# Optimization experiments

Measured on AMD Instinct MI355X. Metric: run time of the kernel, lower is better.

## Reference

```python
import jax, jax.numpy as jnp
import numpy as np


def setup_inputs() -> dict:
    key = jax.random.key(0)
    k1, k2, k3, k4, k5 = jax.random.split(key, 5)
    N, C, H, W = 1, 256, 336, 336
    R, P = 256, 7
    features = jax.random.normal(k1, (N, C, H, W), dtype=jnp.float32)
    # ROIs: integer [x1, y1, x2, y2]; width/height in [P, 63] so every bin is non-empty,
    # and boxes stay inside the feature map.
    x1 = jax.random.randint(k2, (R,), 0, H - 64)
    y1 = jax.random.randint(k3, (R,), 0, H - 64)
    w = jax.random.randint(k4, (R,), P, 64)
    h = jax.random.randint(k5, (R,), P, 64)
    rois = jnp.stack([x1, y1, x1 + w, y1 + h], axis=1).astype(jnp.int32)
    return {"features": features, "rois": rois, "output_size": P}


def _bin_index(lo, size, P, L):
    """For each roi, map every coordinate in [0, L) to its bin index in [0, P), or P if outside.

    Boundaries replicate: int(x1 + (width / P) * w) with float32 division and
    truncation (coords are non-negative, so trunc == floor).
    lo, size: [R] float32.  Returns [R, L] int32.
    """
    ws = jnp.arange(P + 1, dtype=jnp.float32)
    b = jnp.floor(lo[:, None] + (size / P)[:, None] * ws[None, :]).astype(jnp.int32)  # [R, P+1]
    j = jnp.arange(L, dtype=jnp.int32)
    # bin index = number of interior boundaries b[1..P] that are <= j
    cnt = jnp.sum((j[None, None, :] >= b[:, 1:, None]).astype(jnp.int32), axis=1)  # [R, L]
    return jnp.where(j[None, :] < b[:, :1], P, cnt)


def reference(features, rois, output_size):
    P = output_size
    feat = features[0]  # [C, H, W]  (original code requires N == 1)
    C, H, W = feat.shape
    x1 = rois[:, 0].astype(jnp.float32)
    y1 = rois[:, 1].astype(jnp.float32)
    rw = jnp.maximum(rois[:, 2] - rois[:, 0] + 1, 1).astype(jnp.float32)
    rh = jnp.maximum(rois[:, 3] - rois[:, 1] + 1, 1).astype(jnp.float32)
    col_bin = _bin_index(x1, rw, P, W)  # [R, W]
    row_bin = _bin_index(y1, rh, P, H)  # [R, H]

    def pool_one(cb, rb):
        # reduce columns into width-bins: [W, C, H] -> [P+1, C, H], drop 'outside' segment
        t = jax.ops.segment_max(jnp.moveaxis(feat, 2, 0), cb, num_segments=P + 1)[:P]  # [Pw, C, H]
        # reduce rows into height-bins: [H, Pw, C] -> [P+1, Pw, C]
        t = jax.ops.segment_max(jnp.moveaxis(t, 2, 0), rb, num_segments=P + 1)[:P]  # [Ph, Pw, C]
        return jnp.transpose(t, (2, 0, 1))  # [C, Ph, Pw]

    return jax.vmap(pool_one)(col_bin, row_bin)  # [R, C, P, P]
```

## Files before the change

kernel.cpp:

```cpp
#include <hip/hip_runtime.h>
#include <math.h>


#define POOL_P 7

__device__ __forceinline__ float4 max4(float4 a, float4 b) {
  return make_float4(fmaxf(a.x, b.x), fmaxf(a.y, b.y),
                     fmaxf(a.z, b.z), fmaxf(a.w, b.w));
}

__global__ __launch_bounds__(128) void roipool_kernel(
    const float* __restrict__ feat, const int* __restrict__ rois,
    float* __restrict__ out, int C, int H, int W, int R) {
  const int x  = blockIdx.x & 7;
  const int s  = blockIdx.x >> 3;
  const int pass = s / R;
  const int r    = s - pass * R;
  const int cg8  = (pass << 3) | x;

  const int wid  = threadIdx.x >> 6;
  const int lane = threadIdx.x & 63;
  const int k  = lane >> 4;
  const int li = lane & 15;
  const int c0 = (cg8 << 3) + (wid << 2);

  const int4 roi = *reinterpret_cast<const int4*>(rois + 4 * r);
  const int x1 = roi.x, y1 = roi.y;
  const int rw = max(roi.z - x1 + 1, 1);
  const int rh = max(roi.w - y1 + 1, 1);
  const int x2 = x1 + rw - 1;

  const float sx = __fdiv_rn((float)rw, (float)POOL_P);
  const float sy = __fdiv_rn((float)rh, (float)POOL_P);
  const float x1f = (float)x1, y1f = (float)y1;

  const int xa = x1 & ~3;
  const bool tailc = (x2 >= xa + 64);

  const int lslot = min((x2 - xa) >> 2, 15);
  const int lic = min(li, lslot);

  const size_t HW = (size_t)H * W;
  const float* fck = feat + (size_t)(c0 + k) * HW;
  const float* pm  = fck + xa + (lic << 2);
  const float* pt  = fck + xa + 64;

  __shared__ float stg[2][POOL_P][4][72];
  extern __shared__ float lds_pad[];

  const float NEG = -__builtin_inff();

#pragma unroll
  for (int ph = 0; ph < POOL_P; ++ph) {
    const int h0   = (int)__fadd_rn(y1f, __fmul_rn(sy, (float)ph));
    const int hend = (int)__fadd_rn(y1f, __fmul_rn(sy, (float)(ph + 1)));
    const int hl = hend - 1;
    float4 m  = make_float4(NEG, NEG, NEG, NEG);
    float4 tm = m;
    for (int h = h0; h < hend; h += 4) {
      const int o1 = (min(h + 1, hl) - h) * W;
      const int o2 = (min(h + 2, hl) - h) * W;
      const int o3 = (min(h + 3, hl) - h) * W;
      const float* p = pm + (size_t)h * W;
      float4 v0 = *reinterpret_cast<const float4*>(p);
      float4 v1 = *reinterpret_cast<const float4*>(p + o1);
      float4 v2 = *reinterpret_cast<const float4*>(p + o2);
      float4 v3 = *reinterpret_cast<const float4*>(p + o3);
      m = max4(m, max4(max4(v0, v1), max4(v2, v3)));
      if (tailc && li == 0) {
        const float* q = pt + (size_t)h * W;
        float4 t0 = *reinterpret_cast<const float4*>(q);
        float4 t1 = *reinterpret_cast<const float4*>(q + o1);
        float4 t2 = *reinterpret_cast<const float4*>(q + o2);
        float4 t3 = *reinterpret_cast<const float4*>(q + o3);
        tm = max4(tm, max4(max4(t0, t1), max4(t2, t3)));
      }
    }
    float* sp = &stg[wid][ph][k][0];
    *reinterpret_cast<float4*>(sp + (li << 2)) = m;
    if (tailc && li == 0) *reinterpret_cast<float4*>(sp + 64) = tm;
  }

  const size_t ob = ((size_t)r * C + c0) * (POOL_P * POOL_P);
#pragma unroll
  for (int i = lane; i < 4 * POOL_P * POOL_P; i += 64) {
    const int k2 = i / (POOL_P * POOL_P);
    const int j  = i - k2 * (POOL_P * POOL_P);
    const int ph = j / POOL_P;
    const int pw = j - ph * POOL_P;
    const int w0 = (int)__fadd_rn(x1f, __fmul_rn(sx, (float)pw)) - xa;
    const int w1 = (int)__fadd_rn(x1f, __fmul_rn(sx, (float)(pw + 1))) - xa;
    const float* sq = &stg[wid][ph][k2][0];
    float m = NEG;
    for (int w = w0; w < w1; ++w) m = fmaxf(m, sq[w]);
    out[ob + i] = m;
  }
}

extern "C" void kernel_launch(void* const* d_in, const int* in_sizes, int n_in,
                              void* d_out, int out_size, void* d_ws, size_t ws_size,
                              hipStream_t stream) {
  const float* feat = (const float*)d_in[0];
  const int*   rois = (const int*)d_in[1];
  float*       out  = (float*)d_out;

  const int C = 256, H = 336, W = 336;
  const int R = in_sizes[1] / 4;

  const int n_cg8 = C / 8;
  dim3 grid(n_cg8 * R), block(128);
  roipool_kernel<<<grid, block, 3072, stream>>>(feat, rois, out, C, H, W, R);
}
```

Measured before the change: 54.31 us.

## Split blocks into single-wave workgroups and hoist tail-column loads out of row loop

Each 128-thread block handling two 4-channel groups becomes two 64-thread blocks, doubling the grid and dropping the padded dynamic LDS allocation. The row loop now advances float4 pointers with constant row strides hardcoded for W=336, and a separate remainder step replaces per-iteration min() offset clamping. The tail-column loads handled by lane 0 move into their own loop after the main pass, so the main loop carries no divergent branch. The hardcoded strides tie the kernel to W=336.

```diff
diff --git a/kernel.cpp b/kernel.cpp
--- a/kernel.cpp
+++ b/kernel.cpp
@@ -9,20 +9,21 @@
                      fmaxf(a.z, b.z), fmaxf(a.w, b.w));
 }
 
-__global__ __launch_bounds__(128) void roipool_kernel(
+__global__ __launch_bounds__(64) void roipool_kernel(
     const float* __restrict__ feat, const int* __restrict__ rois,
     float* __restrict__ out, int C, int H, int W, int R) {
   const int x  = blockIdx.x & 7;
   const int s  = blockIdx.x >> 3;
-  const int pass = s / R;
-  const int r    = s - pass * R;
+  const int pass = s / (2 * R);
+  const int t    = s - pass * 2 * R;
+  const int r    = t >> 1;
+  const int half = t & 1;
   const int cg8  = (pass << 3) | x;
 
-  const int wid  = threadIdx.x >> 6;
-  const int lane = threadIdx.x & 63;
+  const int lane = threadIdx.x;
   const int k  = lane >> 4;
   const int li = lane & 15;
-  const int c0 = (cg8 << 3) + (wid << 2);
+  const int c0 = (cg8 << 3) + (half << 2);
 
   const int4 roi = *reinterpret_cast<const int4*>(rois + 4 * r);
   const int x1 = roi.x, y1 = roi.y;
@@ -41,12 +42,12 @@
   const int lic = min(li, lslot);
 
   const size_t HW = (size_t)H * W;
+  const int W4 = W >> 2;
   const float* fck = feat + (size_t)(c0 + k) * HW;
-  const float* pm  = fck + xa + (lic << 2);
+  const float4* pmb = reinterpret_cast<const float4*>(fck + xa) + lic;
   const float* pt  = fck + xa + 64;
 
-  __shared__ float stg[2][POOL_P][4][72];
-  extern __shared__ float lds_pad[];
+  __shared__ float stg[4][POOL_P][72];
 
   const float NEG = -__builtin_inff();
 
@@ -54,31 +55,39 @@
   for (int ph = 0; ph < POOL_P; ++ph) {
     const int h0   = (int)__fadd_rn(y1f, __fmul_rn(sy, (float)ph));
     const int hend = (int)__fadd_rn(y1f, __fmul_rn(sy, (float)(ph + 1)));
-    const int hl = hend - 1;
-    float4 m  = make_float4(NEG, NEG, NEG, NEG);
-    float4 tm = m;
-    for (int h = h0; h < hend; h += 4) {
-      const int o1 = (min(h + 1, hl) - h) * W;
-      const int o2 = (min(h + 2, hl) - h) * W;
-      const int o3 = (min(h + 3, hl) - h) * W;
-      const float* p = pm + (size_t)h * W;
-      float4 v0 = *reinterpret_cast<const float4*>(p);
-      float4 v1 = *reinterpret_cast<const float4*>(p + o1);
-      float4 v2 = *reinterpret_cast<const float4*>(p + o2);
-      float4 v3 = *reinterpret_cast<const float4*>(p + o3);
+    const int cnt = hend - h0;
+    const float4* p4 = pmb + (size_t)h0 * W4;
+    float4 m = make_float4(NEG, NEG, NEG, NEG);
+    for (int it = cnt >> 2; it > 0; --it) {
+      float4 v0 = p4[0];
+      float4 v1 = p4[84];
+      float4 v2 = p4[168];
+      float4 v3 = p4[252];
       m = max4(m, max4(max4(v0, v1), max4(v2, v3)));
-      if (tailc && li == 0) {
-        const float* q = pt + (size_t)h * W;
-        float4 t0 = *reinterpret_cast<const float4*>(q);
-        float4 t1 = *reinterpret_cast<const float4*>(q + o1);
-        float4 t2 = *reinterpret_cast<const float4*>(q + o2);
-        float4 t3 = *reinterpret_cast<const float4*>(q + o3);
-        tm = max4(tm, max4(max4(t0, t1), max4(t2, t3)));
-      }
+      p4 += 336;
     }
-    float* sp = &stg[wid][ph][k][0];
-    *reinterpret_cast<float4*>(sp + (li << 2)) = m;
-    if (tailc && li == 0) *reinterpret_cast<float4*>(sp + 64) = tm;
+    const int rem = cnt & 3;
+    if (rem) {
+      const int o1 = (rem > 1) ? 84 : 0;
+      const int o2 = (rem > 2) ? 168 : o1;
+      float4 v0 = p4[0];
+      float4 v1 = p4[o1];
+      float4 v2 = p4[o2];
+      m = max4(m, max4(v0, max4(v1, v2)));
+    }
+    *reinterpret_cast<float4*>(&stg[k][ph][li << 2]) = m;
+  }
+
+  if (tailc && li == 0) {
+#pragma unroll
+    for (int ph = 0; ph < POOL_P; ++ph) {
+      const int h0   = (int)__fadd_rn(y1f, __fmul_rn(sy, (float)ph));
+      const int hend = (int)__fadd_rn(y1f, __fmul_rn(sy, (float)(ph + 1)));
+      float4 tm = make_float4(NEG, NEG, NEG, NEG);
+      for (int h = h0; h < hend; ++h)
+        tm = max4(tm, *reinterpret_cast<const float4*>(pt + (size_t)h * W));
+      *reinterpret_cast<float4*>(&stg[k][ph][64]) = tm;
+    }
   }
 
   const size_t ob = ((size_t)r * C + c0) * (POOL_P * POOL_P);
@@ -90,7 +99,7 @@
     const int pw = j - ph * POOL_P;
     const int w0 = (int)__fadd_rn(x1f, __fmul_rn(sx, (float)pw)) - xa;
     const int w1 = (int)__fadd_rn(x1f, __fmul_rn(sx, (float)(pw + 1))) - xa;
-    const float* sq = &stg[wid][ph][k2][0];
+    const float* sq = &stg[k2][ph][0];
     float m = NEG;
     for (int w = w0; w < w1; ++w) m = fmaxf(m, sq[w]);
     out[ob + i] = m;
@@ -108,6 +117,6 @@
   const int R = in_sizes[1] / 4;
 
   const int n_cg8 = C / 8;
-  dim3 grid(n_cg8 * R), block(128);
-  roipool_kernel<<<grid, block, 3072, stream>>>(feat, rois, out, C, H, W, R);
+  dim3 grid(n_cg8 * R * 2), block(64);
+  roipool_kernel<<<grid, block, 0, stream>>>(feat, rois, out, C, H, W, R);
 }
```

New measurement: 52.63 us. 1.03x faster.
